# Kernel optimization log

Hardware: AMD Instinct MI355X
Metric: run time of the kernel (lower is better)

## Reference

```python
import jax, jax.numpy as jnp
import numpy as np

EPS = 1e-3  # Keras BatchNormalization default epsilon
HEADS = 4
KEY_DEPTH = 16   # k
INTRA = 1        # u
VAL_DEPTH = 64   # v = kernel_out // heads = 256 // 4
C_IN = 256
B, HH, WW = 16, 32, 32
N = HH * WW      # == size of positional embedding


def setup_inputs() -> dict:
    key = jax.random.key(0)
    ks = jax.random.split(key, 6)
    x = jax.random.normal(ks[0], (B, HH, WW, C_IN), dtype=jnp.float32)
    # 1x1 conv kernels == dense matrices over the channel dim
    Wq = jax.random.normal(ks[1], (C_IN, KEY_DEPTH * HEADS), dtype=jnp.float32) * 0.05
    Wk = jax.random.normal(ks[2], (C_IN, KEY_DEPTH * INTRA), dtype=jnp.float32) * 0.05
    Wv = jax.random.normal(ks[3], (C_IN, VAL_DEPTH * INTRA), dtype=jnp.float32) * 0.05
    # BatchNorm (inference mode) parameters
    gamma_q = jnp.ones((KEY_DEPTH * HEADS,), jnp.float32)
    beta_q = jnp.zeros((KEY_DEPTH * HEADS,), jnp.float32)
    mean_q = jnp.zeros((KEY_DEPTH * HEADS,), jnp.float32)
    var_q = jnp.ones((KEY_DEPTH * HEADS,), jnp.float32)
    gamma_v = jnp.ones((VAL_DEPTH * INTRA,), jnp.float32)
    beta_v = jnp.zeros((VAL_DEPTH * INTRA,), jnp.float32)
    mean_v = jnp.zeros((VAL_DEPTH * INTRA,), jnp.float32)
    var_v = jnp.ones((VAL_DEPTH * INTRA,), jnp.float32)
    # Positional embedding: [size, size, key_depth, intra_depth], uniform init
    E = jax.random.uniform(ks[4], (N, N, KEY_DEPTH, INTRA), dtype=jnp.float32)
    return {
        'x': x, 'Wq': Wq, 'Wk': Wk, 'Wv': Wv,
        'gamma_q': gamma_q, 'beta_q': beta_q, 'mean_q': mean_q, 'var_q': var_q,
        'gamma_v': gamma_v, 'beta_v': beta_v, 'mean_v': mean_v, 'var_v': var_v,
        'E': E,
    }


def _bn(t, gamma, beta, mean, var):
    return gamma * (t - mean) / jnp.sqrt(var + EPS) + beta


def reference(x, Wq, Wk, Wv, gamma_q, beta_q, mean_q, var_q,
              gamma_v, beta_v, mean_v, var_v, E):
    b, hh, ww, _ = x.shape
    n = hh * ww
    # 1x1 conv projections (context c == x)
    q = jnp.einsum('bhwc,cd->bhwd', x, Wq)           # [b,hh,ww,h*k]
    k = jnp.einsum('bhwc,cd->bhwd', x, Wk)           # [b,hh,ww,u*k]
    v = jnp.einsum('bhwc,cd->bhwd', x, Wv)           # [b,hh,ww,u*v]
    q = _bn(q, gamma_q, beta_q, mean_q, var_q)
    v = _bn(v, gamma_v, beta_v, mean_v, var_v)
    # softmax over the channel axis (faithful to the source code)
    k = jax.nn.softmax(k, axis=-1)
    # rearranges: b hh ww (h k) -> b h k n ; b hh ww (u k) -> b u k n ; b hh ww (u v) -> b u v n
    q = q.reshape(b, n, HEADS, KEY_DEPTH).transpose(0, 2, 3, 1)   # [b,h,k,n]
    k = k.reshape(b, n, INTRA, KEY_DEPTH).transpose(0, 2, 3, 1)   # [b,u,k,n]
    v = v.reshape(b, n, INTRA, VAL_DEPTH).transpose(0, 2, 3, 1)   # [b,u,v,n]
    # content lambda: sum over intra-depth and positions
    lam_c = jnp.einsum('bukn,buvn->bkv', k, v)                    # [b,k,v]
    Yc = jnp.einsum('bhkn,bkv->bhvn', q, lam_c)                   # [b,h,v,n]
    # positional lambdas: E[n,m,k,u] contracted with v[b,u,v,m]
    lam_p = jnp.einsum('nmku,buvm->bnkv', E, v)                   # [b,n,k,v]
    Yp = jnp.einsum('bhkn,bnkv->bhvn', q, lam_p)                  # [b,h,v,n]
    Y = Yc + Yp                                                    # [b,h,v,n]
    # b h v n -> b hh ww (h v)
    out = Y.transpose(0, 3, 1, 2).reshape(b, hh, ww, HEADS * VAL_DEPTH)
    return out
```

## Files before the change

kernel.cpp:

```cpp
#include <hip/hip_runtime.h>
#include <stdint.h>

#define EPS 1e-3f

typedef __bf16 bf16x8 __attribute__((ext_vector_type(8)));
typedef float  f32x4  __attribute__((ext_vector_type(4)));

static __device__ __forceinline__ uint16_t f2bf(float f) {
  union { float f; uint32_t u; } v; v.f = f;
  uint32_t u = v.u;
  uint32_t r = u + 0x7fffu + ((u >> 16) & 1u);
  return (uint16_t)(r >> 16);
}
static __device__ __forceinline__ void gload_lds16(const void* g, void* l) {
  __builtin_amdgcn_global_load_lds(
      (const __attribute__((address_space(1))) unsigned int*)g,
      (__attribute__((address_space(3))) unsigned int*)l, 16, 0, 0);
}

__global__ __launch_bounds__(256) void econv(
    const float* __restrict__ E, uint16_t* __restrict__ Ebf,
    const float* __restrict__ Wq, const float* __restrict__ Wk,
    const float* __restrict__ Wv, uint16_t* __restrict__ WtP)
{
  const int n = blockIdx.x, t = threadIdx.x;
  if (n < 144) {
    const int col = n;
    float val = (col < 64) ? Wq[t * 64 + col]
              : (col < 80) ? Wk[t * 16 + (col - 64)]
                           : Wv[t * 64 + (col - 80)];
    WtP[col * 264 + t] = f2bf(val);
  }
  const float* En = E + (size_t)n * 16384;
#pragma unroll 1
  for (int kq = 0; kq < 4; ++kq) {
#pragma unroll
    for (int mi = 0; mi < 4; ++mi) {
      int m = mi * 256 + t;
      float4 d = *(const float4*)&En[m * 16 + kq * 4];
      const float* dp = (const float*)&d;
#pragma unroll
      for (int j = 0; j < 4; ++j) {
        int k = kq * 4 + j;
        Ebf[(size_t)(n * 16 + k) * 1024 + m] = f2bf(dp[j]);
      }
    }
  }
}

__global__ __launch_bounds__(256) void proj_mfma(
    const float* __restrict__ x, const uint16_t* __restrict__ WtP,
    const float* __restrict__ gq, const float* __restrict__ bq,
    const float* __restrict__ mq, const float* __restrict__ vq,
    const float* __restrict__ gv, const float* __restrict__ bv,
    const float* __restrict__ mv, const float* __restrict__ vvp,
    float* __restrict__ Qf, uint16_t* __restrict__ VbfT,
    float* __restrict__ part)
{
  __shared__ __align__(16) char smem[111616];
  uint16_t* const xA = (uint16_t*)smem;
  char* const Wt = smem + 33792;

  const int t = threadIdx.x;
  const int wid = t >> 6, lane = t & 63;
  const int bid = blockIdx.x;
  const int b = bid >> 4, mc = bid & 15;
  const int r0 = b * 1024 + mc * 64;

#pragma unroll
  for (int i = 0; i < 19; ++i) {
    int off = (i * 256 + t) * 16;
    gload_lds16((const char*)WtP + off, Wt + off);
  }
  {
    const int row = t >> 2, ks0 = (t & 3) * 64;
    const float* src = x + (size_t)(r0 + row) * 256 + ks0;
    uint16_t* dstp = xA + row * 264 + ks0;
#pragma unroll
    for (int i = 0; i < 8; ++i) {
      float4 d0 = *(const float4*)(src + i * 8);
      float4 d1 = *(const float4*)(src + i * 8 + 4);
      union { uint16_t u[8]; uint4 q; } pk;
      pk.u[0] = f2bf(d0.x); pk.u[1] = f2bf(d0.y);
      pk.u[2] = f2bf(d0.z); pk.u[3] = f2bf(d0.w);
      pk.u[4] = f2bf(d1.x); pk.u[5] = f2bf(d1.y);
      pk.u[6] = f2bf(d1.z); pk.u[7] = f2bf(d1.w);
      *(uint4*)(dstp + i * 8) = pk.q;
    }
  }
  __syncthreads();

  f32x4 acc[9];
#pragma unroll
  for (int f = 0; f < 9; ++f) acc[f] = f32x4{0.f, 0.f, 0.f, 0.f};
  const int arow = wid * 16 + (lane & 15);
#pragma unroll
  for (int kst = 0; kst < 8; ++kst) {
    const int sb = kst * 64 + ((lane >> 4) << 4);
    bf16x8 af = *(const bf16x8*)((const char*)xA + arow * 528 + sb);
#pragma unroll
    for (int f = 0; f < 9; ++f) {
      const int crow = f * 16 + (lane & 15);
      bf16x8 bfr = *(const bf16x8*)(Wt + crow * 528 + sb);
      acc[f] = __builtin_amdgcn_mfma_f32_16x16x32_bf16(af, bfr, acc[f], 0, 0, 0);
    }
  }

  const int cl = lane & 15;
  const int rbase = wid * 16 + ((lane >> 4) << 2);

  float qs[4], qb[4], qm[4], vs[4], vb[4], vm[4];
#pragma unroll
  for (int f = 0; f < 4; ++f) {
    const int c = f * 16 + cl;
    qs[f] = gq[c] * rsqrtf(vq[c] + EPS); qb[f] = bq[c]; qm[f] = mq[c];
    vs[f] = gv[c] * rsqrtf(vvp[c] + EPS); vb[f] = bv[c]; vm[f] = mv[c];
  }
#pragma unroll
  for (int f = 0; f < 4; ++f)
#pragma unroll
    for (int r = 0; r < 4; ++r)
      Qf[(size_t)(r0 + rbase + r) * 64 + f * 16 + cl] =
          (acc[f][r] - qm[f]) * qs[f] + qb[f];
  float ex[4];
#pragma unroll
  for (int r = 0; r < 4; ++r) {
    float kv = acc[4][r];
    float mx = kv;
#pragma unroll
    for (int d = 1; d < 16; d <<= 1) mx = fmaxf(mx, __shfl_xor(mx, d, 64));
    float e = __expf(kv - mx);
    float sm = e;
#pragma unroll
    for (int d = 1; d < 16; d <<= 1) sm += __shfl_xor(sm, d, 64);
    ex[r] = e / sm;
  }
  float vv[4][4];
#pragma unroll
  for (int f = 0; f < 4; ++f)
#pragma unroll
    for (int r = 0; r < 4; ++r)
      vv[f][r] = (acc[5 + f][r] - vm[f]) * vs[f] + vb[f];

  __syncthreads();
  float* const vt = (float*)smem;
  float* const ks = (float*)(smem + 64 * 65 * 4);
#pragma unroll
  for (int r = 0; r < 4; ++r) ks[(rbase + r) * 20 + cl] = ex[r];
#pragma unroll
  for (int f = 0; f < 4; ++f)
#pragma unroll
    for (int r = 0; r < 4; ++r) vt[(rbase + r) * 65 + f * 16 + cl] = vv[f][r];
  __syncthreads();

  {
    const int v = t & 63, grp = t >> 6;
#pragma unroll
    for (int h = 0; h < 2; ++h) {
      union { uint16_t u16[8]; uint4 q; } pk;
#pragma unroll
      for (int i = 0; i < 8; ++i)
        pk.u16[i] = f2bf(vt[(grp * 16 + h * 8 + i) * 65 + v]);
      *(uint4*)&VbfT[(size_t)(b * 64 + v) * 1024 + mc * 64 + grp * 16 + h * 8] = pk.q;
    }
  }
  {
    const int kq = t >> 6, v = t & 63;
    float a0 = 0.f, a1 = 0.f, a2 = 0.f, a3 = 0.f;
#pragma unroll 4
    for (int m = 0; m < 64; ++m) {
      float vvx = vt[m * 65 + v];
      a0 = fmaf(ks[m * 20 + kq * 4 + 0], vvx, a0);
      a1 = fmaf(ks[m * 20 + kq * 4 + 1], vvx, a1);
      a2 = fmaf(ks[m * 20 + kq * 4 + 2], vvx, a2);
      a3 = fmaf(ks[m * 20 + kq * 4 + 3], vvx, a3);
    }
    float* dst = part + ((size_t)(b * 16 + mc) << 10) + (kq * 4) * 64 + v;
    dst[0] = a0; dst[64] = a1; dst[128] = a2; dst[192] = a3;
  }
}

__global__ __launch_bounds__(256) void lamc_reduce(const float* __restrict__ part,
                                                   float* __restrict__ Lc)
{
  const int gid = blockIdx.x * 256 + threadIdx.x;
  const int b = gid >> 10, r = gid & 1023;
  const float* p = part + ((size_t)b << 14) + r;
  float s = 0.f;
#pragma unroll
  for (int mc = 0; mc < 16; ++mc) s += p[mc << 10];
  Lc[((size_t)b << 10) + r] = s;
}

__global__ __launch_bounds__(512, 2) void gemm_out(
    const uint16_t* __restrict__ Ebf,
    const uint16_t* __restrict__ VbfT,
    const float* __restrict__ Qf,
    const float* __restrict__ Lc,
    float* __restrict__ out)
{
  __shared__ __align__(16) char smem[131072];
  char* const A0 = smem;
  char* const B0 = smem + 32768;
  char* const A1 = smem + 65536;
  char* const B1 = smem + 98304;

  const int t = threadIdx.x;
  const int wid = t >> 6, lane = t & 63;
  const int wm = wid >> 2, wn = wid & 3;
  const int bid = blockIdx.x;
  const int xcd = bid & 7, idx = bid >> 3;
  const int rb = xcd * 8 + (idx >> 2);
  const int cb = idx & 3;
  const int row0 = rb * 256;
  const int col0 = cb * 256;

  const uint16_t* aptr[4];
  const uint16_t* bptr[4];
  int dst[4];
  {
    const uint16_t* Ab = Ebf + ((size_t)row0 << 10);
    const uint16_t* Bb = VbfT + ((size_t)col0 << 10);
#pragma unroll
    for (int it = 0; it < 4; ++it) {
      int id = it * 512 + t;
      int row = id >> 3, seg = id & 7;
      int src = (row << 10) + ((seg ^ (row & 7)) << 3);
      aptr[it] = Ab + src;
      bptr[it] = Bb + src;
      dst[it] = id * 16;
    }
  }

  f32x4 acc[8][4];
#pragma unroll
  for (int i = 0; i < 8; ++i)
#pragma unroll
    for (int j = 0; j < 4; ++j) acc[i][j] = f32x4{0.f, 0.f, 0.f, 0.f};

#pragma unroll
  for (int it = 0; it < 4; ++it) {
    gload_lds16(aptr[it], A0 + dst[it]);
    gload_lds16(bptr[it], B0 + dst[it]);
  }
  __syncthreads();

#pragma unroll 1
  for (int kt = 0; kt < 16; ++kt) {
    char* Ac = (kt & 1) ? A1 : A0;
    char* Bc = (kt & 1) ? B1 : B0;
    char* An = (kt & 1) ? A0 : A1;
    char* Bn = (kt & 1) ? B0 : B1;
    if (kt < 15) {
      const int off = (kt + 1) * 64;
#pragma unroll
      for (int it = 0; it < 4; ++it) {
        gload_lds16(aptr[it] + off, An + dst[it]);
        gload_lds16(bptr[it] + off, Bn + dst[it]);
      }
    }
    __builtin_amdgcn_s_setprio(1);
#pragma unroll
    for (int kk = 0; kk < 2; ++kk) {
      bf16x8 a[8], b[4];
      const int s = kk * 4 + (lane >> 4);
#pragma unroll
      for (int i = 0; i < 8; ++i) {
        int row = wm * 128 + i * 16 + (lane & 15);
        a[i] = *(const bf16x8*)(Ac + row * 128 + ((s ^ (row & 7)) << 4));
      }
#pragma unroll
      for (int j = 0; j < 4; ++j) {
        int row = wn * 64 + j * 16 + (lane & 15);
        b[j] = *(const bf16x8*)(Bc + row * 128 + ((s ^ (row & 7)) << 4));
      }
#pragma unroll
      for (int i = 0; i < 8; ++i)
#pragma unroll
        for (int j = 0; j < 4; ++j)
          acc[i][j] = __builtin_amdgcn_mfma_f32_16x16x32_bf16(a[i], b[j], acc[i][j], 0, 0, 0);
    }
    __builtin_amdgcn_s_setprio(0);
    __syncthreads();
  }

  float* Cs = (float*)smem;
  const int n0 = rb * 16;
  const int b0 = cb * 4;
#pragma unroll
  for (int p = 0; p < 4; ++p) {
    if (wm == (p >> 1)) {
#pragma unroll
      for (int il = 0; il < 4; ++il) {
        const int i = ((p & 1) << 2) + il;
#pragma unroll
        for (int j = 0; j < 4; ++j) {
          const int col = wn * 64 + j * 16 + (lane & 15);
          const int bb = b0 + (col >> 6), v = col & 63;
#pragma unroll
          for (int r = 0; r < 4; ++r) {
            const int rl = il * 16 + ((lane >> 4) << 2) + r;
            const int k = rl & 15;
            Cs[rl * 258 + col] = acc[i][j][r] + Lc[(size_t)(((bb << 4) + k) << 6) + v];
          }
        }
      }
    }
    __syncthreads();
    {
      const int v = t & 63;
#pragma unroll
      for (int c = 0; c < 8; ++c) {
        const int combo = (wid << 3) + c;
        const int n_l = combo >> 4;
        const int b_l = (combo >> 2) & 3;
        const int h = combo & 3;
        const int n = n0 + (p << 2) + n_l;
        const int bb = b0 + b_l;
        const float* qp = Qf + (((size_t)(bb << 10) + n) << 6) + (h << 4);
        float sum = 0.f;
#pragma unroll
        for (int k = 0; k < 16; ++k)
          sum = fmaf(qp[k], Cs[((n_l << 4) + k) * 258 + (b_l << 6) + v], sum);
        out[(((size_t)(bb << 10) + n) << 8) + (h << 6) + v] = sum;
      }
    }
    __syncthreads();
  }
}

extern "C" void kernel_launch(void* const* d_in, const int* in_sizes, int n_in,
                              void* d_out, int out_size, void* d_ws, size_t ws_size,
                              hipStream_t stream) {
  const float* x   = (const float*)d_in[0];
  const float* Wq  = (const float*)d_in[1];
  const float* Wk  = (const float*)d_in[2];
  const float* Wv  = (const float*)d_in[3];
  const float* gq  = (const float*)d_in[4];
  const float* bq  = (const float*)d_in[5];
  const float* mq  = (const float*)d_in[6];
  const float* vq  = (const float*)d_in[7];
  const float* gv  = (const float*)d_in[8];
  const float* bv  = (const float*)d_in[9];
  const float* mv  = (const float*)d_in[10];
  const float* vvp = (const float*)d_in[11];
  const float* E   = (const float*)d_in[12];
  float* out = (float*)d_out;

  char* ws = (char*)d_ws;
  uint16_t* Ebf  = (uint16_t*)(ws);
  uint16_t* VbfT = (uint16_t*)(ws + 33554432);
  float*    Qf   = (float*)(ws + 35651584);
  float*    part = (float*)(ws + 39845888);
  float*    Lc   = (float*)(ws + 40894464);
  uint16_t* WtP  = (uint16_t*)(ws + 40960000);

  hipLaunchKernelGGL(econv, dim3(1024), dim3(256), 0, stream,
                     E, Ebf, Wq, Wk, Wv, WtP);
  hipLaunchKernelGGL(proj_mfma, dim3(256), dim3(256), 0, stream, x, WtP,
                     gq, bq, mq, vq, gv, bv, mv, vvp, Qf, VbfT, part);
  hipLaunchKernelGGL(lamc_reduce, dim3(64), dim3(256), 0, stream, part, Lc);
  hipLaunchKernelGGL(gemm_out, dim3(256), dim3(512), 0, stream, Ebf, VbfT, Qf, Lc, out);
}
```

Before: 83.59 us.

## Transpose E through LDS, use hardware bf16 converts, finer-grained gemm waits

The E conversion kernel now loads E with fully coalesced float4 reads into an LDS tile, then writes transposed bf16 rows as 16-byte vector stores. Before, each thread issued scattered 2-byte stores. The weight packing moves into its own small kernel. The manual bf16 rounding is replaced by the compiler's __bf16 conversion with paired packing, and the output GEMM swaps its full __syncthreads for explicit vmcnt waits plus raw barriers so the next tile's loads overlap compute. Risks are LDS bank conflicts in the strided transpose reads, one extra kernel launch, and that the vmcnt count must match the issued loads.

```diff
diff --git a/kernel.cpp b/kernel.cpp
--- a/kernel.cpp
+++ b/kernel.cpp
@@ -7,10 +7,12 @@
 typedef float  f32x4  __attribute__((ext_vector_type(4)));
 
 static __device__ __forceinline__ uint16_t f2bf(float f) {
-  union { float f; uint32_t u; } v; v.f = f;
-  uint32_t u = v.u;
-  uint32_t r = u + 0x7fffu + ((u >> 16) & 1u);
-  return (uint16_t)(r >> 16);
+  union { __bf16 b; uint16_t u; } r; r.b = (__bf16)f; return r.u;
+}
+static __device__ __forceinline__ uint32_t cvt2(float lo, float hi) {
+  union { __bf16 b[2]; uint32_t u; } r;
+  r.b[0] = (__bf16)lo; r.b[1] = (__bf16)hi;
+  return r.u;
 }
 static __device__ __forceinline__ void gload_lds16(const void* g, void* l) {
   __builtin_amdgcn_global_load_lds(
@@ -18,33 +20,41 @@
       (__attribute__((address_space(3))) unsigned int*)l, 16, 0, 0);
 }
 
-__global__ __launch_bounds__(256) void econv(
-    const float* __restrict__ E, uint16_t* __restrict__ Ebf,
+__global__ __launch_bounds__(256) void wprep(
     const float* __restrict__ Wq, const float* __restrict__ Wk,
     const float* __restrict__ Wv, uint16_t* __restrict__ WtP)
 {
+  const int col = blockIdx.x, t = threadIdx.x;
+  float val = (col < 64) ? Wq[t * 64 + col]
+            : (col < 80) ? Wk[t * 16 + (col - 64)]
+                         : Wv[t * 64 + (col - 80)];
+  WtP[col * 264 + t] = f2bf(val);
+}
+
+__global__ __launch_bounds__(256) void econv(const float* __restrict__ E,
+                                             uint16_t* __restrict__ Ebf)
+{
+  __shared__ uint16_t lds[1024 * 20 + 8];
   const int n = blockIdx.x, t = threadIdx.x;
-  if (n < 144) {
-    const int col = n;
-    float val = (col < 64) ? Wq[t * 64 + col]
-              : (col < 80) ? Wk[t * 16 + (col - 64)]
-                           : Wv[t * 64 + (col - 80)];
-    WtP[col * 264 + t] = f2bf(val);
-  }
   const float* En = E + (size_t)n * 16384;
-#pragma unroll 1
-  for (int kq = 0; kq < 4; ++kq) {
-#pragma unroll
-    for (int mi = 0; mi < 4; ++mi) {
-      int m = mi * 256 + t;
-      float4 d = *(const float4*)&En[m * 16 + kq * 4];
-      const float* dp = (const float*)&d;
-#pragma unroll
-      for (int j = 0; j < 4; ++j) {
-        int k = kq * 4 + j;
-        Ebf[(size_t)(n * 16 + k) * 1024 + m] = f2bf(dp[j]);
-      }
-    }
+#pragma unroll
+  for (int i = 0; i < 16; ++i) {
+    int f4 = i * 256 + t;
+    float4 d = *(const float4*)(En + (size_t)f4 * 4);
+    int m = f4 >> 2, k0 = (f4 & 3) * 4;
+    uint2 w; w.x = cvt2(d.x, d.y); w.y = cvt2(d.z, d.w);
+    *(uint2*)&lds[m * 20 + k0] = w;
+  }
+  __syncthreads();
+  const int k = t & 15, mg = t >> 4;
+  uint16_t* dst = Ebf + (size_t)(n * 16 + k) * 1024 + mg * 64;
+  const uint16_t* src = lds + (mg * 64) * 20 + k;
+#pragma unroll
+  for (int s = 0; s < 8; ++s) {
+    union { uint16_t u[8]; uint4 q; } pk;
+#pragma unroll
+    for (int j = 0; j < 8; ++j) pk.u[j] = src[(s * 8 + j) * 20];
+    *(uint4*)(dst + s * 8) = pk.q;
   }
 }
 
@@ -80,12 +90,10 @@
     for (int i = 0; i < 8; ++i) {
       float4 d0 = *(const float4*)(src + i * 8);
       float4 d1 = *(const float4*)(src + i * 8 + 4);
-      union { uint16_t u[8]; uint4 q; } pk;
-      pk.u[0] = f2bf(d0.x); pk.u[1] = f2bf(d0.y);
-      pk.u[2] = f2bf(d0.z); pk.u[3] = f2bf(d0.w);
-      pk.u[4] = f2bf(d1.x); pk.u[5] = f2bf(d1.y);
-      pk.u[6] = f2bf(d1.z); pk.u[7] = f2bf(d1.w);
-      *(uint4*)(dstp + i * 8) = pk.q;
+      uint4 q;
+      q.x = cvt2(d0.x, d0.y); q.y = cvt2(d0.z, d0.w);
+      q.z = cvt2(d1.x, d1.y); q.w = cvt2(d1.z, d1.w);
+      *(uint4*)(dstp + i * 8) = q;
     }
   }
   __syncthreads();
@@ -157,11 +165,12 @@
     const int v = t & 63, grp = t >> 6;
 #pragma unroll
     for (int h = 0; h < 2; ++h) {
-      union { uint16_t u16[8]; uint4 q; } pk;
-#pragma unroll
-      for (int i = 0; i < 8; ++i)
-        pk.u16[i] = f2bf(vt[(grp * 16 + h * 8 + i) * 65 + v]);
-      *(uint4*)&VbfT[(size_t)(b * 64 + v) * 1024 + mc * 64 + grp * 16 + h * 8] = pk.q;
+      uint4 q;
+      q.x = cvt2(vt[(grp * 16 + h * 8 + 0) * 65 + v], vt[(grp * 16 + h * 8 + 1) * 65 + v]);
+      q.y = cvt2(vt[(grp * 16 + h * 8 + 2) * 65 + v], vt[(grp * 16 + h * 8 + 3) * 65 + v]);
+      q.z = cvt2(vt[(grp * 16 + h * 8 + 4) * 65 + v], vt[(grp * 16 + h * 8 + 5) * 65 + v]);
+      q.w = cvt2(vt[(grp * 16 + h * 8 + 6) * 65 + v], vt[(grp * 16 + h * 8 + 7) * 65 + v]);
+      *(uint4*)&VbfT[(size_t)(b * 64 + v) * 1024 + mc * 64 + grp * 16 + h * 8] = q;
     }
   }
   {
@@ -214,6 +223,7 @@
   const int cb = idx & 3;
   const int row0 = rb * 256;
   const int col0 = cb * 256;
+  const int n0 = rb * 16;
 
   const uint16_t* aptr[4];
   const uint16_t* bptr[4];
@@ -243,7 +253,6 @@
     gload_lds16(aptr[it], A0 + dst[it]);
     gload_lds16(bptr[it], B0 + dst[it]);
   }
-  __syncthreads();
 
 #pragma unroll 1
   for (int kt = 0; kt < 16; ++kt) {
@@ -258,7 +267,12 @@
         gload_lds16(aptr[it] + off, An + dst[it]);
         gload_lds16(bptr[it] + off, Bn + dst[it]);
       }
-    }
+      asm volatile("s_waitcnt vmcnt(8)" ::: "memory");
+    } else {
+      asm volatile("s_waitcnt vmcnt(0)" ::: "memory");
+    }
+    __builtin_amdgcn_s_barrier();
+    __builtin_amdgcn_sched_barrier(0);
     __builtin_amdgcn_s_setprio(1);
 #pragma unroll
     for (int kk = 0; kk < 2; ++kk) {
@@ -281,11 +295,11 @@
           acc[i][j] = __builtin_amdgcn_mfma_f32_16x16x32_bf16(a[i], b[j], acc[i][j], 0, 0, 0);
     }
     __builtin_amdgcn_s_setprio(0);
-    __syncthreads();
-  }
+    __builtin_amdgcn_s_barrier();
+  }
+  __syncthreads();
 
   float* Cs = (float*)smem;
-  const int n0 = rb * 16;
   const int b0 = cb * 4;
 #pragma unroll
   for (int p = 0; p < 4; ++p) {
@@ -355,8 +369,8 @@
   float*    Lc   = (float*)(ws + 40894464);
   uint16_t* WtP  = (uint16_t*)(ws + 40960000);
 
-  hipLaunchKernelGGL(econv, dim3(1024), dim3(256), 0, stream,
-                     E, Ebf, Wq, Wk, Wv, WtP);
+  hipLaunchKernelGGL(wprep, dim3(144), dim3(256), 0, stream, Wq, Wk, Wv, WtP);
+  hipLaunchKernelGGL(econv, dim3(1024), dim3(256), 0, stream, E, Ebf);
   hipLaunchKernelGGL(proj_mfma, dim3(256), dim3(256), 0, stream, x, WtP,
                      gq, bq, mq, vq, gv, bv, mv, vvp, Qf, VbfT, part);
   hipLaunchKernelGGL(lamc_reduce, dim3(64), dim3(256), 0, stream, part, Lc);
```

New measurement: 86.85 us. 3.9% more time.
